# Performance work log

Measured on AMD Instinct MI355X. Metric: run time of the kernel, lower is better.

Reference implementation:

```python
import jax, jax.numpy as jnp
import numpy as np

B, N, M, J, D, PF = 4, 131072, 10475, 55, 64, 486


def setup_inputs() -> dict:
    key = jax.random.key(0)
    ks = jax.random.split(key, 16)
    return {
        "pts": jax.random.normal(ks[0], (B, N, 3), jnp.float32),
        "betas": jax.random.normal(ks[1], (B, 10), jnp.float32),
        "pose_feature": jax.random.normal(ks[2], (B, PF), jnp.float32),
        "init_spdir": jax.random.normal(ks[3], (M, 3, 10), jnp.float32),
        "init_podir": jax.random.normal(ks[4], (PF, 3 * M), jnp.float32),
        "init_faces": jax.random.randint(ks[5], (N, 3), 0, M, jnp.int32),
        "tfs_A": jax.random.normal(ks[6], (B, J, 4, 4), jnp.float32),
        "tfs_inv": jax.random.normal(ks[7], (1, J, 4, 4), jnp.float32),
        "poseoff_cano": jax.random.normal(ks[8], (1, N, 3), jnp.float32),
        "lbsw": jax.random.uniform(ks[9], (1, N, J), jnp.float32),
        "lbs_voxel": jax.random.uniform(ks[10], (1, J, D, D, D), jnp.float32),
        "vox_scale": jnp.ones((1, 1, 3), jnp.float32),
        "vox_offset": jnp.zeros((1, 1, 3), jnp.float32),
        "mask": jax.random.randint(ks[11], (B, N), 0, 2, jnp.int32),
    }


def _trilinear(vox, x, scale, offset):
    # vox: [J,D,D,D], x: [b,n,3] -> [b,n,J] trilinearly interpolated weights
    nj, nd = vox.shape[0], vox.shape[-1]
    g = jnp.clip(x * scale + offset, -1.0, 1.0)          # normalized coords
    t = (g + 1.0) * 0.5 * (nd - 1)                        # voxel coords
    i0 = jnp.clip(jnp.floor(t), 0, nd - 2).astype(jnp.int32)
    f = t - i0                                            # fractional part
    vf = vox.reshape(nj, -1)                              # [J, D^3]
    out = jnp.zeros(x.shape[:-1] + (nj,), x.dtype)
    for dx in (0, 1):
        for dy in (0, 1):
            for dz in (0, 1):
                ix = i0[..., 0] + dx
                iy = i0[..., 1] + dy
                iz = i0[..., 2] + dz
                wgt = ((f[..., 0] if dx else 1.0 - f[..., 0]) *
                       (f[..., 1] if dy else 1.0 - f[..., 1]) *
                       (f[..., 2] if dz else 1.0 - f[..., 2]))
                fid = (ix * nd + iy) * nd + iz            # flat voxel index [b,n]
                out = out + wgt[..., None] * jnp.moveaxis(vf[:, fid], 0, -1)
    return out


def reference(pts, betas, pose_feature, init_spdir, init_podir, init_faces,
              tfs_A, tfs_inv, poseoff_cano, lbsw, lbs_voxel, vox_scale,
              vox_offset, mask):
    b, n, _ = pts.shape
    # blend-shape offsets on template vertices
    shape_full = jnp.einsum('bl,mkl->bmk', betas, init_spdir)      # [b,M,3]
    pose_full = (pose_feature @ init_podir).reshape(b, -1, 3)      # [b,M,3]
    # face-vertex gather then average over the 3 vertices of each face
    shape_off = shape_full[:, init_faces].mean(axis=2)             # [b,F,3]
    pose_off = pose_full[:, init_faces].mean(axis=2)               # [b,F,3]
    x = pts + shape_off + pose_off - poseoff_cano                  # canonical pts + offsets
    # voxel-grid skinning-weight lookup at canonical points
    w_vox = _trilinear(lbs_voxel[0], pts, vox_scale, vox_offset)   # [b,n,J]
    w = jnp.where(mask[..., None] > 0, lbsw, w_vox)
    w = w / jnp.clip(w.sum(-1, keepdims=True), 1e-8)
    # per-point blended transforms: A @ A_inv_template
    tfs = tfs_A @ tfs_inv                                          # [b,J,4,4]
    T = jnp.einsum('bnj,bjrc->bnrc', w, tfs)                       # [b,n,4,4]
    xh = jnp.concatenate([x, jnp.ones_like(x[..., :1])], axis=-1)
    posed = jnp.einsum('bnrc,bnc->bnr', T, xh)[..., :3]
    return posed.reshape(b, n, 1, 3), T
```

## Files before the change

### kernel.cpp

```cpp
#include <hip/hip_runtime.h>

#define B_  4
#define N_  131072
#define J_  55
#define JP_ 56
#define D_  64
#define D3_ 262144
#define PF_ 486
#define COLS_ 31425

#define BL16(u) __uint_as_float((u) << 16)
#define BH16(u) __uint_as_float((u) & 0xffff0000u)

typedef float vfloat4 __attribute__((ext_vector_type(4)));

__device__ __forceinline__ unsigned short f2bf(float v) {
    unsigned u = __float_as_uint(v);
    u += 0x7fffu + ((u >> 16) & 1u);
    return (unsigned short)(u >> 16);
}

__global__ void k_off_pose(const float* __restrict__ pf,
                           const float* __restrict__ podir,
                           const float* __restrict__ betas,
                           const float* __restrict__ spdir,
                           float* __restrict__ off_full) {
    int col = blockIdx.x * 256 + threadIdx.x;
    if (col >= COLS_) return;
    int pc = blockIdx.y;
    float a0 = 0.f, a1 = 0.f, a2 = 0.f, a3 = 0.f;
    if (pc == 0) {
        float sp[10];
#pragma unroll
        for (int l = 0; l < 10; ++l) sp[l] = spdir[col * 10 + l];
#pragma unroll
        for (int l = 0; l < 10; ++l) {
            a0 += betas[0 * 10 + l] * sp[l];
            a1 += betas[1 * 10 + l] * sp[l];
            a2 += betas[2 * 10 + l] * sp[l];
            a3 += betas[3 * 10 + l] * sp[l];
        }
    }
    int p0 = pc * 61;
    int p1 = p0 + 61; if (p1 > PF_) p1 = PF_;
    int p = p0;
    for (; p + 4 <= p1; p += 4) {
        float v0 = podir[(size_t)(p + 0) * COLS_ + col];
        float v1 = podir[(size_t)(p + 1) * COLS_ + col];
        float v2 = podir[(size_t)(p + 2) * COLS_ + col];
        float v3 = podir[(size_t)(p + 3) * COLS_ + col];
        a0 += pf[0 * PF_ + p] * v0 + pf[0 * PF_ + p + 1] * v1 +
              pf[0 * PF_ + p + 2] * v2 + pf[0 * PF_ + p + 3] * v3;
        a1 += pf[1 * PF_ + p] * v0 + pf[1 * PF_ + p + 1] * v1 +
              pf[1 * PF_ + p + 2] * v2 + pf[1 * PF_ + p + 3] * v3;
        a2 += pf[2 * PF_ + p] * v0 + pf[2 * PF_ + p + 1] * v1 +
              pf[2 * PF_ + p + 2] * v2 + pf[2 * PF_ + p + 3] * v3;
        a3 += pf[3 * PF_ + p] * v0 + pf[3 * PF_ + p + 1] * v1 +
              pf[3 * PF_ + p + 2] * v2 + pf[3 * PF_ + p + 3] * v3;
    }
    for (; p < p1; ++p) {
        float v = podir[(size_t)p * COLS_ + col];
        a0 += pf[0 * PF_ + p] * v;
        a1 += pf[1 * PF_ + p] * v;
        a2 += pf[2 * PF_ + p] * v;
        a3 += pf[3 * PF_ + p] * v;
    }
    atomicAdd(&off_full[0 * COLS_ + col], a0);
    atomicAdd(&off_full[1 * COLS_ + col], a1);
    atomicAdd(&off_full[2 * COLS_ + col], a2);
    atomicAdd(&off_full[3 * COLS_ + col], a3);
}

__global__ void k_tfs(const float* __restrict__ A,
                      const float* __restrict__ Ainv,
                      float* __restrict__ tfsP) {
    int tid = blockIdx.x * 256 + threadIdx.x;
    if (tid >= B_ * JP_ * 16) return;
    int rc = tid & 15;
    int jb = tid >> 4;
    int j = jb % JP_;
    int b = jb / JP_;
    float v = 0.f;
    if (j < J_) {
        int r = rc >> 2, c = rc & 3;
#pragma unroll
        for (int k = 0; k < 4; ++k)
            v += A[((b * J_ + j) * 4 + r) * 4 + k] * Ainv[(j * 4 + k) * 4 + c];
    }
    tfsP[tid] = v;
}

__global__ __launch_bounds__(256) void k_G(
    const float* __restrict__ vox, const float* __restrict__ tfsP,
    uint4* __restrict__ Gtb, float* __restrict__ Stb) {
    int v = blockIdx.x * 256 + threadIdx.x;
    float g[4][16];
    float s = 0.f;
#pragma unroll
    for (int b = 0; b < 4; ++b)
#pragma unroll
        for (int r = 0; r < 16; ++r) g[b][r] = 0.f;
    for (int j0 = 0; j0 < J_; j0 += 5) {
        float wv[5];
#pragma unroll
        for (int k = 0; k < 5; ++k)
            wv[k] = vox[(size_t)(j0 + k) * D3_ + v];
#pragma unroll
        for (int k = 0; k < 5; ++k) {
            float w = wv[k];
            s += w;
#pragma unroll
            for (int b = 0; b < 4; ++b) {
                const float* tr = tfsP + (b * JP_ + j0 + k) * 16;
#pragma unroll
                for (int r = 0; r < 16; ++r) g[b][r] += w * tr[r];
            }
        }
    }
    Stb[v] = s;
#pragma unroll
    for (int b = 0; b < 4; ++b) {
        unsigned gw[8];
#pragma unroll
        for (int k = 0; k < 8; ++k)
            gw[k] = (unsigned)f2bf(g[b][2 * k]) |
                    ((unsigned)f2bf(g[b][2 * k + 1]) << 16);
        uint4* gp = Gtb + ((size_t)b * D3_ + v) * 2;
        gp[0] = make_uint4(gw[0], gw[1], gw[2], gw[3]);
        gp[1] = make_uint4(gw[4], gw[5], gw[6], gw[7]);
    }
}

#define ACC8(Toff, qa, qb)                                 \
    T[Toff + 0] += w0 * BL16(qa.x) + w1 * BL16(qb.x);      \
    T[Toff + 1] += w0 * BH16(qa.x) + w1 * BH16(qb.x);      \
    T[Toff + 2] += w0 * BL16(qa.y) + w1 * BL16(qb.y);      \
    T[Toff + 3] += w0 * BH16(qa.y) + w1 * BH16(qb.y);      \
    T[Toff + 4] += w0 * BL16(qa.z) + w1 * BL16(qb.z);      \
    T[Toff + 5] += w0 * BH16(qa.z) + w1 * BH16(qb.z);      \
    T[Toff + 6] += w0 * BL16(qa.w) + w1 * BL16(qb.w);      \
    T[Toff + 7] += w0 * BH16(qa.w) + w1 * BH16(qb.w);

__global__ __launch_bounds__(256) void k_main(
    const float* __restrict__ pts, const int* __restrict__ faces,
    const float* __restrict__ poseoff, const int* __restrict__ mask,
    const float* __restrict__ vox_scale, const float* __restrict__ vox_offset,
    const float* __restrict__ off_full, const float* __restrict__ tfsP,
    const float* __restrict__ lbsw, const uint4* __restrict__ Gtb,
    const float* __restrict__ Stb,
    float* __restrict__ out_posed, float* __restrict__ out_T) {
    __shared__ float sx0[256], sx1[256], sx2[256];
    __shared__ float sf0[256], sf1[256], sf2[256];
    __shared__ int   scell[256];
    __shared__ unsigned short lst[256];
    __shared__ int wc[4];

    int bid = blockIdx.x;
    int b  = (bid >> 1) & 3;
    int nc = ((bid >> 3) << 1) | (bid & 1);
    int tid = threadIdx.x;
    int n = nc * 256 + tid;
    int i = (b << 17) | n;

    float px = pts[3 * i + 0], py = pts[3 * i + 1], pz = pts[3 * i + 2];
    int f0 = faces[3 * n + 0], f1 = faces[3 * n + 1], f2 = faces[3 * n + 2];
    const float* ob = off_full + b * COLS_;
    const float c3 = 1.f / 3.f;
    float ox = (ob[f0 * 3 + 0] + ob[f1 * 3 + 0] + ob[f2 * 3 + 0]) * c3;
    float oy = (ob[f0 * 3 + 1] + ob[f1 * 3 + 1] + ob[f2 * 3 + 1]) * c3;
    float oz = (ob[f0 * 3 + 2] + ob[f1 * 3 + 2] + ob[f2 * 3 + 2]) * c3;
    sx0[tid] = px + ox - poseoff[3 * n + 0];
    sx1[tid] = py + oy - poseoff[3 * n + 1];
    sx2[tid] = pz + oz - poseoff[3 * n + 2];

    bool isv = !(mask[i] > 0);
    if (isv) {
        float sxc = vox_scale[0], syc = vox_scale[1], szc = vox_scale[2];
        float o0 = vox_offset[0], o1 = vox_offset[1], o2 = vox_offset[2];
        float gx = fminf(fmaxf(px * sxc + o0, -1.f), 1.f);
        float gy = fminf(fmaxf(py * syc + o1, -1.f), 1.f);
        float gz = fminf(fmaxf(pz * szc + o2, -1.f), 1.f);
        float tx = (gx + 1.f) * 0.5f * (D_ - 1);
        float ty = (gy + 1.f) * 0.5f * (D_ - 1);
        float tz = (gz + 1.f) * 0.5f * (D_ - 1);
        int ix = (int)floorf(tx); if (ix > D_ - 2) ix = D_ - 2; if (ix < 0) ix = 0;
        int iy = (int)floorf(ty); if (iy > D_ - 2) iy = D_ - 2; if (iy < 0) iy = 0;
        int iz = (int)floorf(tz); if (iz > D_ - 2) iz = D_ - 2; if (iz < 0) iz = 0;
        sf0[tid] = tx - ix;
        sf1[tid] = ty - iy;
        sf2[tid] = tz - iz;
        scell[tid] = (ix * D_ + iy) * D_ + iz;
    }

    unsigned long long bal = __ballot(isv);
    int lane = tid & 63, wid = tid >> 6;
    if (lane == 0) wc[wid] = __popcll(bal);
    __syncthreads();
    int pre = 0;
#pragma unroll
    for (int k = 0; k < 4; ++k) pre += (k < wid) ? wc[k] : 0;
    int tot = wc[0] + wc[1] + wc[2] + wc[3];
    unsigned long long lt = ((unsigned long long)1 << lane) - 1ull;
    int vbefore = pre + __popcll(bal & lt);
    int pos = isv ? vbefore : (tot + (tid - vbefore));
    lst[pos] = (unsigned short)tid;
    __syncthreads();

    int slot = lst[tid];
    float x0 = sx0[slot], x1 = sx1[slot], x2 = sx2[slot];
    int ii = (b << 17) | (nc * 256 + slot);

    float T[16];
#pragma unroll
    for (int r = 0; r < 16; ++r) T[r] = 0.f;
    float wsum = 0.f;

    if (tid < tot) {
        float fx = sf0[slot], fy = sf1[slot], fz = sf2[slot];
        int cell = scell[slot];
        const uint4* Gb = Gtb + (size_t)b * D3_ * 2;
#pragma unroll
        for (int cc = 0; cc < 4; ++cc) {
            int fid = cell + ((cc & 2) ? D_ * D_ : 0) + ((cc & 1) ? D_ : 0);
            float wxy = ((cc & 2) ? fx : 1.f - fx) * ((cc & 1) ? fy : 1.f - fy);
            float w0 = wxy * (1.f - fz);
            float w1 = wxy * fz;
            const uint4* R = Gb + (size_t)fid * 2;
            uint4 q0 = R[0], q1 = R[1], q2 = R[2], q3 = R[3];
            wsum += w0 * Stb[fid] + w1 * Stb[fid + 1];
            ACC8(0, q0, q2)
            ACC8(8, q1, q3)
        }
    } else {
        int n2 = nc * 256 + slot;
        const float* lw = lbsw + (size_t)n2 * J_;
        const float* tb = tfsP + b * (JP_ * 16);
        float wv[8];
        for (int c = 0; c < 6; ++c) {
#pragma unroll
            for (int k = 0; k < 8; ++k) wv[k] = lw[c * 8 + k];
#pragma unroll
            for (int k = 0; k < 8; ++k) {
                float w = wv[k];
                wsum += w;
                const float* tr = tb + (c * 8 + k) * 16;
#pragma unroll
                for (int r = 0; r < 16; ++r) T[r] += w * tr[r];
            }
        }
#pragma unroll
        for (int k = 0; k < 7; ++k) wv[k] = lw[48 + k];
#pragma unroll
        for (int k = 0; k < 7; ++k) {
            float w = wv[k];
            wsum += w;
            const float* tr = tb + (48 + k) * 16;
#pragma unroll
            for (int r = 0; r < 16; ++r) T[r] += w * tr[r];
        }
    }

    float inv = 1.f / fmaxf(wsum, 1e-8f);
    float t[16];
#pragma unroll
    for (int r = 0; r < 16; ++r) t[r] = T[r] * inv;
    out_posed[3 * ii + 0] = t[0] * x0 + t[1] * x1 + t[2] * x2 + t[3];
    out_posed[3 * ii + 1] = t[4] * x0 + t[5] * x1 + t[6] * x2 + t[7];
    out_posed[3 * ii + 2] = t[8] * x0 + t[9] * x1 + t[10] * x2 + t[11];
    vfloat4* to = (vfloat4*)(out_T + (size_t)ii * 16);
    vfloat4 r0 = { t[0], t[1], t[2], t[3] };
    vfloat4 r1 = { t[4], t[5], t[6], t[7] };
    vfloat4 r2 = { t[8], t[9], t[10], t[11] };
    vfloat4 r3 = { t[12], t[13], t[14], t[15] };
    __builtin_nontemporal_store(r0, to + 0);
    __builtin_nontemporal_store(r1, to + 1);
    __builtin_nontemporal_store(r2, to + 2);
    __builtin_nontemporal_store(r3, to + 3);
}

extern "C" void kernel_launch(void* const* d_in, const int* in_sizes, int n_in,
                              void* d_out, int out_size, void* d_ws, size_t ws_size,
                              hipStream_t stream) {
    const float* pts      = (const float*)d_in[0];
    const float* betas    = (const float*)d_in[1];
    const float* pf       = (const float*)d_in[2];
    const float* spdir    = (const float*)d_in[3];
    const float* podir    = (const float*)d_in[4];
    const int*   faces    = (const int*)d_in[5];
    const float* tfs_A    = (const float*)d_in[6];
    const float* tfs_inv  = (const float*)d_in[7];
    const float* poseoff  = (const float*)d_in[8];
    const float* lbsw     = (const float*)d_in[9];
    const float* vox      = (const float*)d_in[10];
    const float* vscale   = (const float*)d_in[11];
    const float* voffset  = (const float*)d_in[12];
    const int*   mask     = (const int*)d_in[13];

    char* w = (char*)d_ws;
    uint4* Gtb      = (uint4*)w;
    float* Stb      = (float*)(w + 33554432);
    float* off_full = (float*)(w + 34603008);
    float* tfsP     = (float*)(w + 35106048);

    float* out_posed = (float*)d_out;
    float* out_T     = out_posed + (size_t)B_ * N_ * 3;

    (void)hipMemsetAsync(off_full, 0, 503040, stream);
    k_tfs<<<(B_ * JP_ * 16 + 255) / 256, 256, 0, stream>>>(tfs_A, tfs_inv, tfsP);
    k_G<<<D3_ / 256, 256, 0, stream>>>(vox, tfsP, Gtb, Stb);
    dim3 gpose((COLS_ + 255) / 256, 8);
    k_off_pose<<<gpose, 256, 0, stream>>>(pf, podir, betas, spdir, off_full);

    k_main<<<2048, 256, 0, stream>>>(pts, faces, poseoff, mask, vscale, voffset,
                                     off_full, tfsP, lbsw, Gtb, Stb,
                                     out_posed, out_T);
}
```

Measured before the change: 293.5 us.

## Fuse prelude kernels, pack lbsw to bf16, stage outputs via LDS

Merges the memset and tfs kernels into one launch, and the voxel-G, pose-offset GEMV and a new lbsw-to-bf16 packing pass into a single multi-role prelude kernel. The pose GEMV gets finer p-chunks with 8-wide loads, and the G loop gains software prefetch. k_main reads packed bf16 lbsw with vector loads and stages results in shared memory so output writes are coalesced in original point order rather than compacted order. The packing pass adds an extra read and write of lbsw each call and lowers weight precision to bf16. The larger shared buffer may reduce occupancy.

New measurement: 292.7 us. No clear change (-0.3%).

```diff
diff --git a/kernel.cpp b/kernel.cpp
--- a/kernel.cpp
+++ b/kernel.cpp
@@ -9,6 +9,10 @@
 #define PF_ 486
 #define COLS_ 31425
 
+#define GZ_ 1024
+#define OZ_ 1968
+#define PZ_ 14336
+
 #define BL16(u) __uint_as_float((u) << 16)
 #define BH16(u) __uint_as_float((u) & 0xffff0000u)
 
@@ -20,114 +24,138 @@
     return (unsigned short)(u >> 16);
 }
 
-__global__ void k_off_pose(const float* __restrict__ pf,
-                           const float* __restrict__ podir,
-                           const float* __restrict__ betas,
-                           const float* __restrict__ spdir,
-                           float* __restrict__ off_full) {
-    int col = blockIdx.x * 256 + threadIdx.x;
-    if (col >= COLS_) return;
-    int pc = blockIdx.y;
-    float a0 = 0.f, a1 = 0.f, a2 = 0.f, a3 = 0.f;
-    if (pc == 0) {
-        float sp[10];
-#pragma unroll
-        for (int l = 0; l < 10; ++l) sp[l] = spdir[col * 10 + l];
-#pragma unroll
-        for (int l = 0; l < 10; ++l) {
-            a0 += betas[0 * 10 + l] * sp[l];
-            a1 += betas[1 * 10 + l] * sp[l];
-            a2 += betas[2 * 10 + l] * sp[l];
-            a3 += betas[3 * 10 + l] * sp[l];
-        }
-    }
-    int p0 = pc * 61;
-    int p1 = p0 + 61; if (p1 > PF_) p1 = PF_;
-    int p = p0;
-    for (; p + 4 <= p1; p += 4) {
-        float v0 = podir[(size_t)(p + 0) * COLS_ + col];
-        float v1 = podir[(size_t)(p + 1) * COLS_ + col];
-        float v2 = podir[(size_t)(p + 2) * COLS_ + col];
-        float v3 = podir[(size_t)(p + 3) * COLS_ + col];
-        a0 += pf[0 * PF_ + p] * v0 + pf[0 * PF_ + p + 1] * v1 +
-              pf[0 * PF_ + p + 2] * v2 + pf[0 * PF_ + p + 3] * v3;
-        a1 += pf[1 * PF_ + p] * v0 + pf[1 * PF_ + p + 1] * v1 +
-              pf[1 * PF_ + p + 2] * v2 + pf[1 * PF_ + p + 3] * v3;
-        a2 += pf[2 * PF_ + p] * v0 + pf[2 * PF_ + p + 1] * v1 +
-              pf[2 * PF_ + p + 2] * v2 + pf[2 * PF_ + p + 3] * v3;
-        a3 += pf[3 * PF_ + p] * v0 + pf[3 * PF_ + p + 1] * v1 +
-              pf[3 * PF_ + p + 2] * v2 + pf[3 * PF_ + p + 3] * v3;
-    }
-    for (; p < p1; ++p) {
-        float v = podir[(size_t)p * COLS_ + col];
-        a0 += pf[0 * PF_ + p] * v;
-        a1 += pf[1 * PF_ + p] * v;
-        a2 += pf[2 * PF_ + p] * v;
-        a3 += pf[3 * PF_ + p] * v;
-    }
-    atomicAdd(&off_full[0 * COLS_ + col], a0);
-    atomicAdd(&off_full[1 * COLS_ + col], a1);
-    atomicAdd(&off_full[2 * COLS_ + col], a2);
-    atomicAdd(&off_full[3 * COLS_ + col], a3);
-}
-
-__global__ void k_tfs(const float* __restrict__ A,
-                      const float* __restrict__ Ainv,
-                      float* __restrict__ tfsP) {
-    int tid = blockIdx.x * 256 + threadIdx.x;
-    if (tid >= B_ * JP_ * 16) return;
-    int rc = tid & 15;
-    int jb = tid >> 4;
-    int j = jb % JP_;
-    int b = jb / JP_;
-    float v = 0.f;
-    if (j < J_) {
-        int r = rc >> 2, c = rc & 3;
-#pragma unroll
-        for (int k = 0; k < 4; ++k)
-            v += A[((b * J_ + j) * 4 + r) * 4 + k] * Ainv[(j * 4 + k) * 4 + c];
-    }
-    tfsP[tid] = v;
-}
-
-__global__ __launch_bounds__(256) void k_G(
+__global__ __launch_bounds__(256) void k_tfs_zero(
+    const float* __restrict__ A, const float* __restrict__ Ainv,
+    float* __restrict__ tfsP, float4* __restrict__ off_zero) {
+    int bx = blockIdx.x;
+    if (bx < 14) {
+        int tid = bx * 256 + threadIdx.x;
+        int rc = tid & 15;
+        int jb = tid >> 4;
+        int j = jb % JP_;
+        int b = jb / JP_;
+        float v = 0.f;
+        if (j < J_) {
+            int r = rc >> 2, c = rc & 3;
+#pragma unroll
+            for (int k = 0; k < 4; ++k)
+                v += A[((b * J_ + j) * 4 + r) * 4 + k] *
+                     Ainv[(j * 4 + k) * 4 + c];
+        }
+        tfsP[tid] = v;
+    } else {
+        int idx = (bx - 14) * 256 + threadIdx.x;
+        off_zero[idx] = make_float4(0.f, 0.f, 0.f, 0.f);
+    }
+}
+
+__global__ __launch_bounds__(256) void k_prelude(
     const float* __restrict__ vox, const float* __restrict__ tfsP,
-    uint4* __restrict__ Gtb, float* __restrict__ Stb) {
-    int v = blockIdx.x * 256 + threadIdx.x;
-    float g[4][16];
-    float s = 0.f;
-#pragma unroll
-    for (int b = 0; b < 4; ++b)
-#pragma unroll
-        for (int r = 0; r < 16; ++r) g[b][r] = 0.f;
-    for (int j0 = 0; j0 < J_; j0 += 5) {
-        float wv[5];
-#pragma unroll
-        for (int k = 0; k < 5; ++k)
-            wv[k] = vox[(size_t)(j0 + k) * D3_ + v];
-#pragma unroll
-        for (int k = 0; k < 5; ++k) {
-            float w = wv[k];
-            s += w;
-#pragma unroll
-            for (int b = 0; b < 4; ++b) {
-                const float* tr = tfsP + (b * JP_ + j0 + k) * 16;
-#pragma unroll
-                for (int r = 0; r < 16; ++r) g[b][r] += w * tr[r];
-            }
-        }
-    }
-    Stb[v] = s;
-#pragma unroll
-    for (int b = 0; b < 4; ++b) {
-        unsigned gw[8];
-#pragma unroll
-        for (int k = 0; k < 8; ++k)
-            gw[k] = (unsigned)f2bf(g[b][2 * k]) |
-                    ((unsigned)f2bf(g[b][2 * k + 1]) << 16);
-        uint4* gp = Gtb + ((size_t)b * D3_ + v) * 2;
-        gp[0] = make_uint4(gw[0], gw[1], gw[2], gw[3]);
-        gp[1] = make_uint4(gw[4], gw[5], gw[6], gw[7]);
+    uint4* __restrict__ Gtb, float* __restrict__ Stb,
+    const float* __restrict__ pf, const float* __restrict__ podir,
+    const float* __restrict__ betas, const float* __restrict__ spdir,
+    float* __restrict__ off_full,
+    const float* __restrict__ lbsw, unsigned* __restrict__ lbswP32) {
+    int bx = blockIdx.x;
+    int tid = threadIdx.x;
+
+    if (bx < GZ_) {
+        int v = bx * 256 + tid;
+        float g[4][16];
+        float s = 0.f;
+#pragma unroll
+        for (int b = 0; b < 4; ++b)
+#pragma unroll
+            for (int r = 0; r < 16; ++r) g[b][r] = 0.f;
+        float wa[5], wb[5];
+#pragma unroll
+        for (int k = 0; k < 5; ++k) wa[k] = vox[(size_t)k * D3_ + v];
+        for (int j0 = 0; j0 < J_; j0 += 5) {
+            if (j0 + 5 < J_) {
+#pragma unroll
+                for (int k = 0; k < 5; ++k)
+                    wb[k] = vox[(size_t)(j0 + 5 + k) * D3_ + v];
+            }
+#pragma unroll
+            for (int k = 0; k < 5; ++k) {
+                float w = wa[k];
+                s += w;
+#pragma unroll
+                for (int b = 0; b < 4; ++b) {
+                    const float* tr = tfsP + (b * JP_ + j0 + k) * 16;
+#pragma unroll
+                    for (int r = 0; r < 16; ++r) g[b][r] += w * tr[r];
+                }
+            }
+#pragma unroll
+            for (int k = 0; k < 5; ++k) wa[k] = wb[k];
+        }
+        Stb[v] = s;
+#pragma unroll
+        for (int b = 0; b < 4; ++b) {
+            unsigned gw[8];
+#pragma unroll
+            for (int k = 0; k < 8; ++k)
+                gw[k] = (unsigned)f2bf(g[b][2 * k]) |
+                        ((unsigned)f2bf(g[b][2 * k + 1]) << 16);
+            uint4* gp = Gtb + ((size_t)b * D3_ + v) * 2;
+            gp[0] = make_uint4(gw[0], gw[1], gw[2], gw[3]);
+            gp[1] = make_uint4(gw[4], gw[5], gw[6], gw[7]);
+        }
+    } else if (bx < GZ_ + OZ_) {
+        int idx = bx - GZ_;
+        int colb = idx % 123;
+        int pc = idx / 123;
+        int col = colb * 256 + tid;
+        if (col >= COLS_) return;
+        float a0 = 0.f, a1 = 0.f, a2 = 0.f, a3 = 0.f;
+        if (pc == 0) {
+            float sp[10];
+#pragma unroll
+            for (int l = 0; l < 10; ++l) sp[l] = spdir[col * 10 + l];
+#pragma unroll
+            for (int l = 0; l < 10; ++l) {
+                a0 += betas[0 * 10 + l] * sp[l];
+                a1 += betas[1 * 10 + l] * sp[l];
+                a2 += betas[2 * 10 + l] * sp[l];
+                a3 += betas[3 * 10 + l] * sp[l];
+            }
+        }
+        int p0 = pc * 31;
+        int p1 = p0 + 31; if (p1 > PF_) p1 = PF_;
+        int p = p0;
+        for (; p + 8 <= p1; p += 8) {
+            float v8[8];
+#pragma unroll
+            for (int k = 0; k < 8; ++k)
+                v8[k] = podir[(size_t)(p + k) * COLS_ + col];
+#pragma unroll
+            for (int k = 0; k < 8; ++k) {
+                a0 += pf[0 * PF_ + p + k] * v8[k];
+                a1 += pf[1 * PF_ + p + k] * v8[k];
+                a2 += pf[2 * PF_ + p + k] * v8[k];
+                a3 += pf[3 * PF_ + p + k] * v8[k];
+            }
+        }
+        for (; p < p1; ++p) {
+            float v = podir[(size_t)p * COLS_ + col];
+            a0 += pf[0 * PF_ + p] * v;
+            a1 += pf[1 * PF_ + p] * v;
+            a2 += pf[2 * PF_ + p] * v;
+            a3 += pf[3 * PF_ + p] * v;
+        }
+        atomicAdd(&off_full[0 * COLS_ + col], a0);
+        atomicAdd(&off_full[1 * COLS_ + col], a1);
+        atomicAdd(&off_full[2 * COLS_ + col], a2);
+        atomicAdd(&off_full[3 * COLS_ + col], a3);
+    } else {
+        int e = (bx - GZ_ - OZ_) * 256 + tid;
+        int n = e / 28;
+        int jj = e - n * 28;
+        int j0 = 2 * jj;
+        float w0 = lbsw[(size_t)n * J_ + j0];
+        float w1 = (j0 + 1 < J_) ? lbsw[(size_t)n * J_ + j0 + 1] : 0.f;
+        lbswP32[e] = (unsigned)f2bf(w0) | ((unsigned)f2bf(w1) << 16);
     }
 }
 
@@ -146,17 +174,18 @@
     const float* __restrict__ poseoff, const int* __restrict__ mask,
     const float* __restrict__ vox_scale, const float* __restrict__ vox_offset,
     const float* __restrict__ off_full, const float* __restrict__ tfsP,
-    const float* __restrict__ lbsw, const uint4* __restrict__ Gtb,
+    const unsigned short* __restrict__ lbswP, const uint4* __restrict__ Gtb,
     const float* __restrict__ Stb,
     float* __restrict__ out_posed, float* __restrict__ out_T) {
     __shared__ float sx0[256], sx1[256], sx2[256];
     __shared__ float sf0[256], sf1[256], sf2[256];
     __shared__ int   scell[256];
+    __shared__ float sT[256 * 16];
     __shared__ unsigned short lst[256];
     __shared__ int wc[4];
 
     int bid = blockIdx.x;
-    int b  = (bid >> 1) & 3;
+    int b  = (bid & 7) >> 1;
     int nc = ((bid >> 3) << 1) | (bid & 1);
     int tid = threadIdx.x;
     int n = nc * 256 + tid;
@@ -208,7 +237,6 @@
 
     int slot = lst[tid];
     float x0 = sx0[slot], x1 = sx1[slot], x2 = sx2[slot];
-    int ii = (b << 17) | (nc * 256 + slot);
 
     float T[16];
 #pragma unroll
@@ -233,30 +261,26 @@
         }
     } else {
         int n2 = nc * 256 + slot;
-        const float* lw = lbsw + (size_t)n2 * J_;
+        const uint4* lw = (const uint4*)(lbswP + (size_t)n2 * 56);
+        uint4 q[7];
+#pragma unroll
+        for (int k = 0; k < 7; ++k) q[k] = lw[k];
         const float* tb = tfsP + b * (JP_ * 16);
-        float wv[8];
-        for (int c = 0; c < 6; ++c) {
-#pragma unroll
-            for (int k = 0; k < 8; ++k) wv[k] = lw[c * 8 + k];
-#pragma unroll
-            for (int k = 0; k < 8; ++k) {
-                float w = wv[k];
+#pragma unroll
+        for (int k = 0; k < 7; ++k) {
+            float w8[8];
+            w8[0] = BL16(q[k].x); w8[1] = BH16(q[k].x);
+            w8[2] = BL16(q[k].y); w8[3] = BH16(q[k].y);
+            w8[4] = BL16(q[k].z); w8[5] = BH16(q[k].z);
+            w8[6] = BL16(q[k].w); w8[7] = BH16(q[k].w);
+#pragma unroll
+            for (int m = 0; m < 8; ++m) {
+                float w = w8[m];
                 wsum += w;
-                const float* tr = tb + (c * 8 + k) * 16;
+                const float* tr = tb + (k * 8 + m) * 16;
 #pragma unroll
                 for (int r = 0; r < 16; ++r) T[r] += w * tr[r];
             }
-        }
-#pragma unroll
-        for (int k = 0; k < 7; ++k) wv[k] = lw[48 + k];
-#pragma unroll
-        for (int k = 0; k < 7; ++k) {
-            float w = wv[k];
-            wsum += w;
-            const float* tr = tb + (48 + k) * 16;
-#pragma unroll
-            for (int r = 0; r < 16; ++r) T[r] += w * tr[r];
         }
     }
 
@@ -264,18 +288,23 @@
     float t[16];
 #pragma unroll
     for (int r = 0; r < 16; ++r) t[r] = T[r] * inv;
-    out_posed[3 * ii + 0] = t[0] * x0 + t[1] * x1 + t[2] * x2 + t[3];
-    out_posed[3 * ii + 1] = t[4] * x0 + t[5] * x1 + t[6] * x2 + t[7];
-    out_posed[3 * ii + 2] = t[8] * x0 + t[9] * x1 + t[10] * x2 + t[11];
-    vfloat4* to = (vfloat4*)(out_T + (size_t)ii * 16);
-    vfloat4 r0 = { t[0], t[1], t[2], t[3] };
-    vfloat4 r1 = { t[4], t[5], t[6], t[7] };
-    vfloat4 r2 = { t[8], t[9], t[10], t[11] };
-    vfloat4 r3 = { t[12], t[13], t[14], t[15] };
-    __builtin_nontemporal_store(r0, to + 0);
-    __builtin_nontemporal_store(r1, to + 1);
-    __builtin_nontemporal_store(r2, to + 2);
-    __builtin_nontemporal_store(r3, to + 3);
+    sx0[slot] = t[0] * x0 + t[1] * x1 + t[2] * x2 + t[3];
+    sx1[slot] = t[4] * x0 + t[5] * x1 + t[6] * x2 + t[7];
+    sx2[slot] = t[8] * x0 + t[9] * x1 + t[10] * x2 + t[11];
+#pragma unroll
+    for (int r = 0; r < 16; ++r) sT[slot * 16 + r] = t[r];
+    __syncthreads();
+
+    out_posed[3 * i + 0] = sx0[tid];
+    out_posed[3 * i + 1] = sx1[tid];
+    out_posed[3 * i + 2] = sx2[tid];
+    vfloat4* to = (vfloat4*)(out_T + (size_t)i * 16);
+#pragma unroll
+    for (int k = 0; k < 4; ++k) {
+        vfloat4 r = { sT[tid * 16 + 4 * k + 0], sT[tid * 16 + 4 * k + 1],
+                      sT[tid * 16 + 4 * k + 2], sT[tid * 16 + 4 * k + 3] };
+        __builtin_nontemporal_store(r, to + k);
+    }
 }
 
 extern "C" void kernel_launch(void* const* d_in, const int* in_sizes, int n_in,
@@ -297,21 +326,21 @@
     const int*   mask     = (const int*)d_in[13];
 
     char* w = (char*)d_ws;
-    uint4* Gtb      = (uint4*)w;
-    float* Stb      = (float*)(w + 33554432);
-    float* off_full = (float*)(w + 34603008);
-    float* tfsP     = (float*)(w + 35106048);
+    uint4* Gtb              = (uint4*)w;
+    float* Stb              = (float*)(w + 33554432);
+    unsigned short* lbswP   = (unsigned short*)(w + 34603008);
+    float* off_full         = (float*)(w + 49283072);
+    float* tfsP             = (float*)(w + 49799168);
 
     float* out_posed = (float*)d_out;
     float* out_T     = out_posed + (size_t)B_ * N_ * 3;
 
-    (void)hipMemsetAsync(off_full, 0, 503040, stream);
-    k_tfs<<<(B_ * JP_ * 16 + 255) / 256, 256, 0, stream>>>(tfs_A, tfs_inv, tfsP);
-    k_G<<<D3_ / 256, 256, 0, stream>>>(vox, tfsP, Gtb, Stb);
-    dim3 gpose((COLS_ + 255) / 256, 8);
-    k_off_pose<<<gpose, 256, 0, stream>>>(pf, podir, betas, spdir, off_full);
-
-    k_main<<<2048, 256, 0, stream>>>(pts, faces, poseoff, mask, vscale, voffset,
-                                     off_full, tfsP, lbsw, Gtb, Stb,
+    k_tfs_zero<<<137, 256, 0, stream>>>(tfs_A, tfs_inv, tfsP,
+                                        (float4*)off_full);
+    k_prelude<<<GZ_ + OZ_ + PZ_, 256, 0, stream>>>(
+        vox, tfsP, Gtb, Stb, pf, podir, betas, spdir, off_full,
+        lbsw, (unsigned*)lbswP);
+    k_main<<<2048, 256, 0, stream>>>(pts, faces, poseoff, mask, vscale,
+                                     voffset, off_full, tfsP, lbswP, Gtb, Stb,
                                      out_posed, out_T);
 }
```
